# Optimization experiments

Measured on AMD Instinct MI355X. Metric: run time of the kernel, lower is better.

Reference implementation:

```python
import jax, jax.numpy as jnp
import numpy as np
from jax import lax

CENTER_VAR = 0.1
SIZE_VAR = 0.2
CONF_THR = 0.01
NMS_THR = 0.45
NMS_K = 100  # fixed candidate budget per (image, class) for jit-compatible NMS

B, N, C = 32, 24564, 81  # batch, priors (SSD512), classes incl. background


def setup_inputs() -> dict:
    key = jax.random.key(0)
    k1, k2, k3, k4 = jax.random.split(key, 4)
    cls_logits = jax.random.normal(k1, (B, N, C), dtype=jnp.float32)
    bbox_pred = jax.random.normal(k2, (B, N, 4), dtype=jnp.float32)
    # priors in center form (cx, cy, w, h), all in (0, 1)
    centers = jax.random.uniform(k3, (N, 2), dtype=jnp.float32)
    sizes = jax.random.uniform(k4, (N, 2), dtype=jnp.float32, minval=0.02, maxval=0.9)
    priors = jnp.concatenate([centers, sizes], axis=-1)
    return {"cls_logits": cls_logits, "bbox_pred": bbox_pred, "priors": priors}


def decode_boxes(locations, priors):
    # convert_locations_to_boxes (center form)
    cxcy = locations[..., :2] * CENTER_VAR * priors[..., 2:] + priors[..., :2]
    wh = jnp.exp(locations[..., 2:] * SIZE_VAR) * priors[..., 2:]
    # center_form_to_corner_form
    return jnp.concatenate([cxcy - wh / 2, cxcy + wh / 2], axis=-1)


def iou_matrix(boxes):
    # boxes: [K, 4] corner form -> [K, K] IoU
    lt = jnp.maximum(boxes[:, None, :2], boxes[None, :, :2])
    rb = jnp.minimum(boxes[:, None, 2:], boxes[None, :, 2:])
    wh = jnp.clip(rb - lt, 0.0)
    inter = wh[..., 0] * wh[..., 1]
    area = jnp.clip(boxes[:, 2] - boxes[:, 0], 0.0) * jnp.clip(boxes[:, 3] - boxes[:, 1], 0.0)
    return inter / (area[:, None] + area[None, :] - inter + 1e-8)


def greedy_nms(boxes, valid):
    # boxes [K,4] sorted by descending score; valid [K] bool (score > threshold)
    K = boxes.shape[0]
    iou = iou_matrix(boxes)
    idx = jnp.arange(K)

    def body(i, keep):
        suppress = (iou[i] > NMS_THR) & keep[i] & (idx > i)
        return keep & ~suppress

    keep = lax.fori_loop(0, K, body, valid)
    return keep


def reference(cls_logits, bbox_pred, priors):
    scores = jax.nn.softmax(cls_logits, axis=2)            # [B, N, C]
    boxes = decode_boxes(bbox_pred, priors)                # [B, N, 4]

    # --- post-processing: per-class top-k candidates + greedy NMS ---
    fg = jnp.transpose(scores[:, :, 1:], (0, 2, 1))        # [B, C-1, N]
    cand_scores, cand_idx = lax.top_k(fg, NMS_K)           # [B, C-1, K]
    cand_boxes = jnp.take_along_axis(boxes[:, None], cand_idx[..., None], axis=2)  # [B, C-1, K, 4]
    valid = cand_scores > CONF_THR

    keep = jax.vmap(jax.vmap(greedy_nms))(cand_boxes, valid)  # [B, C-1, K] bool
    nms_scores = jnp.where(keep, cand_scores, 0.0)
    nms_boxes = jnp.where(keep[..., None], cand_boxes, 0.0)
    return scores, boxes, nms_scores, nms_boxes, keep
```

## Files before the change

### kernel.cpp

```cpp
#include <hip/hip_runtime.h>
#include <hip/hip_bf16.h>
#include <math.h>

#define BB 32
#define NN 24564
#define CC 81
#define CM1 80
#define KK 100
#define CAP 512
#define CONF 0.01f
#define NMSTHR 0.45f

#define TROWS 64
#define TPB ((NN + TROWS - 1) / TROWS)

__device__ __forceinline__ float fexp_cr(float x) {
    return (float)exp((double)x);
}

__global__ __launch_bounds__(256) void softmax_kernel(const float* __restrict__ logits,
                                                      float* __restrict__ scores,
                                                      float* __restrict__ fg, int use_fg) {
#pragma clang fp contract(off)
    __shared__ __align__(16) float tile[TROWS * CC];
    __shared__ float sres[TROWS];

    const int blk = blockIdx.x;
    const int b = blk / TPB;
    const int t = blk - b * TPB;
    const int n0 = t * TROWS;
    int rows = NN - n0;
    if (rows > TROWS) rows = TROWS;
    const int tid = threadIdx.x;

    const float4* src4 = (const float4*)(logits + ((size_t)b * NN + n0) * CC);
    float4* tile4 = (float4*)tile;
    const int total4 = (rows * CC) >> 2;
    for (int i = tid; i < total4; i += 256) tile4[i] = src4[i];
    __syncthreads();

    if (tid < rows) {
        float* x = tile + tid * CC;
        float m = x[0];
        for (int c = 1; c < CC; ++c) m = fmaxf(m, x[c]);

        float r[8];
#pragma unroll
        for (int j = 0; j < 8; ++j) {
            float e = expf(x[j] - m);
            x[j] = e;
            r[j] = e;
        }
        for (int i = 8; i < 80; i += 8) {
#pragma unroll
            for (int j = 0; j < 8; ++j) {
                float e = expf(x[i + j] - m);
                x[i + j] = e;
                r[j] += e;
            }
        }
        float res = ((r[0] + r[1]) + (r[2] + r[3])) + ((r[4] + r[5]) + (r[6] + r[7]));
        float e80 = expf(x[80] - m);
        x[80] = e80;
        res += e80;
        sres[tid] = res;
    }
    __syncthreads();

    float4* dst4 = (float4*)(scores + ((size_t)b * NN + n0) * CC);
    for (int i = tid; i < total4; i += 256) {
        float4 v = tile4[i];
        int e0 = i << 2;
        unsigned r0 = (unsigned)(e0    ) / 81u;
        unsigned r1 = (unsigned)(e0 + 1) / 81u;
        unsigned r2 = (unsigned)(e0 + 2) / 81u;
        unsigned r3 = (unsigned)(e0 + 3) / 81u;
        v.x = v.x / sres[r0];
        v.y = v.y / sres[r1];
        v.z = v.z / sres[r2];
        v.w = v.w / sres[r3];
        dst4[i] = v;
        tile4[i] = v;
    }
    __syncthreads();

    if (use_fg) {
        const int rows4 = rows >> 2;
        for (int idx = tid; idx < CM1 * (TROWS >> 2); idx += 256) {
            int c  = idx >> 4;
            int j4 = idx & 15;
            if (j4 < rows4) {
                int j = j4 << 2;
                float4 v;
                v.x = tile[(j    ) * CC + (c + 1)];
                v.y = tile[(j + 1) * CC + (c + 1)];
                v.z = tile[(j + 2) * CC + (c + 1)];
                v.w = tile[(j + 3) * CC + (c + 1)];
                *(float4*)(fg + ((size_t)(b * CM1 + c)) * NN + n0 + j) = v;
            }
        }
    }
}

__global__ __launch_bounds__(256) void decode_kernel(const float* __restrict__ loc,
                                                     const float* __restrict__ priors,
                                                     float* __restrict__ boxes) {
#pragma clang fp contract(off)
    int row = blockIdx.x * 256 + threadIdx.x;
    if (row >= BB * NN) return;
    int n = row % NN;
    float4 L = ((const float4*)loc)[row];
    float4 P = ((const float4*)priors)[n];
    float cx = (L.x * 0.1f) * P.z + P.x;
    float cy = (L.y * 0.1f) * P.w + P.y;
    float w  = fexp_cr(L.z * 0.2f) * P.z;
    float h  = fexp_cr(L.w * 0.2f) * P.w;
    float4 o;
    o.x = cx - w * 0.5f;
    o.y = cy - h * 0.5f;
    o.z = cx + w * 0.5f;
    o.w = cy + h * 0.5f;
    ((float4*)boxes)[row] = o;
}

__global__ __launch_bounds__(256) void topk_nms_kernel(
    const float* __restrict__ scores, const float* __restrict__ fg, int use_fg,
    const float* __restrict__ boxes,
    float* __restrict__ nms_scores, float* __restrict__ nms_boxes,
    float* __restrict__ keep_out)
{
#pragma clang fp contract(off)
    const int blk = blockIdx.x;
    const int b = blk / CM1;
    const int c = blk - b * CM1;
    const int tid = threadIdx.x;

    __shared__ unsigned hist[4096];
    __shared__ unsigned partial[256];
    __shared__ unsigned long long cand[CAP];
    __shared__ unsigned scnt;
    __shared__ unsigned s_T;
    __shared__ int s_b1, s_above, s_refine;
    __shared__ float sbx[KK][4];
    __shared__ float sarea[KK];
    __shared__ float sscore[KK];
    __shared__ int skeep[KK];

    const float* src;
    size_t stride;
    if (use_fg) { src = fg + ((size_t)(b * CM1 + c)) * NN; stride = 1; }
    else        { src = scores + ((size_t)b * NN) * CC + (c + 1); stride = CC; }

    for (int i = tid; i < 4096; i += 256) hist[i] = 0u;
    __syncthreads();
    for (int n = tid; n < NN; n += 256) {
        unsigned bits = __float_as_uint(src[(size_t)n * stride]);
        atomicAdd(&hist[bits >> 20], 1u);
    }
    __syncthreads();
    unsigned psum = 0;
    for (int j = 0; j < 16; ++j) psum += hist[tid * 16 + j];
    partial[tid] = psum;
    __syncthreads();
    if (tid == 0) {
        unsigned acc = 0; int b1 = 0;
        for (int t = 255; t >= 0; --t) {
            if (acc + partial[t] >= (unsigned)KK) {
                for (int bin = t * 16 + 15; ; --bin) {
                    if (acc + hist[bin] >= (unsigned)KK) { b1 = bin; break; }
                    acc += hist[bin];
                }
                break;
            }
            acc += partial[t];
        }
        s_b1 = b1;
        s_above = (int)acc;
        s_refine = (acc + hist[b1] > CAP) ? 1 : 0;
        s_T = ((unsigned)b1) << 20;
    }
    __syncthreads();

    if (s_refine) {
        int b1 = s_b1;
        for (int i = tid; i < 4096; i += 256) hist[i] = 0u;
        __syncthreads();
        for (int n = tid; n < NN; n += 256) {
            unsigned bits = __float_as_uint(src[(size_t)n * stride]);
            if ((int)(bits >> 20) == b1) atomicAdd(&hist[(bits >> 8) & 0xFFFu], 1u);
        }
        __syncthreads();
        psum = 0;
        for (int j = 0; j < 16; ++j) psum += hist[tid * 16 + j];
        partial[tid] = psum;
        __syncthreads();
        if (tid == 0) {
            int K2 = KK - s_above;
            unsigned acc = 0; int b2 = 0;
            for (int t = 255; t >= 0; --t) {
                if ((int)(acc + partial[t]) >= K2) {
                    for (int bin = t * 16 + 15; ; --bin) {
                        if ((int)(acc + hist[bin]) >= K2) { b2 = bin; break; }
                        acc += hist[bin];
                    }
                    break;
                }
                acc += partial[t];
            }
            s_T = (((unsigned)s_b1) << 20) | (((unsigned)b2) << 8);
        }
        __syncthreads();
    }

    if (tid == 0) scnt = 0u;
    __syncthreads();
    unsigned T = s_T;
    for (int n = tid; n < NN; n += 256) {
        unsigned bits = __float_as_uint(src[(size_t)n * stride]);
        if (bits >= T) {
            unsigned pos = atomicAdd(&scnt, 1u);
            if (pos < CAP) {
                cand[pos] = (((unsigned long long)bits) << 32)
                          | (unsigned)(0xFFFFFFFFu - (unsigned)n);
            }
        }
    }
    __syncthreads();
    unsigned cnt = scnt; if (cnt > CAP) cnt = CAP;
    for (int i = tid; i < CAP; i += 256) {
        if ((unsigned)i >= cnt) cand[i] = 0ull;
    }
    __syncthreads();

    for (unsigned k = 2; k <= CAP; k <<= 1) {
        for (unsigned j = k >> 1; j > 0; j >>= 1) {
            for (unsigned e = tid; e < CAP; e += 256) {
                unsigned ixj = e ^ j;
                if (ixj > e) {
                    unsigned long long a = cand[e], bb2 = cand[ixj];
                    bool desc = ((e & k) == 0);
                    if (desc ? (a < bb2) : (a > bb2)) { cand[e] = bb2; cand[ixj] = a; }
                }
            }
            __syncthreads();
        }
    }

    if (tid < KK) {
        unsigned long long key = cand[tid];
        unsigned bits = (unsigned)(key >> 32);
        unsigned n = 0xFFFFFFFFu - (unsigned)(key & 0xFFFFFFFFu);
        float s = __uint_as_float(bits);
        sscore[tid] = s;
        skeep[tid] = (s > CONF) ? 1 : 0;
        float4 bx = ((const float4*)boxes)[(size_t)b * NN + n];
        sbx[tid][0] = bx.x; sbx[tid][1] = bx.y; sbx[tid][2] = bx.z; sbx[tid][3] = bx.w;
        sarea[tid] = fmaxf(bx.z - bx.x, 0.f) * fmaxf(bx.w - bx.y, 0.f);
    }
    __syncthreads();

    for (int i = 0; i < KK - 1; ++i) {
        if (skeep[i]) {
            int j = i + 1 + tid;
            if (j < KK) {
                float xx1 = fmaxf(sbx[i][0], sbx[j][0]);
                float yy1 = fmaxf(sbx[i][1], sbx[j][1]);
                float xx2 = fminf(sbx[i][2], sbx[j][2]);
                float yy2 = fminf(sbx[i][3], sbx[j][3]);
                float w = fmaxf(xx2 - xx1, 0.f);
                float h = fmaxf(yy2 - yy1, 0.f);
                float inter = w * h;
                float den = ((sarea[i] + sarea[j]) - inter) + 1e-8f;
                if (inter / den > NMSTHR) skeep[j] = 0;
            }
        }
        __syncthreads();
    }

    if (tid < KK) {
        int kf = skeep[tid];
        size_t oidx = (size_t)blk * KK + tid;
        nms_scores[oidx] = kf ? sscore[tid] : 0.f;
        keep_out[oidx]   = kf ? 1.f : 0.f;
        float4 ob;
        ob.x = kf ? sbx[tid][0] : 0.f;
        ob.y = kf ? sbx[tid][1] : 0.f;
        ob.z = kf ? sbx[tid][2] : 0.f;
        ob.w = kf ? sbx[tid][3] : 0.f;
        ((float4*)nms_boxes)[oidx] = ob;
    }
}

extern "C" void kernel_launch(void* const* d_in, const int* in_sizes, int n_in,
                              void* d_out, int out_size, void* d_ws, size_t ws_size,
                              hipStream_t stream) {
    const float* logits = (const float*)d_in[0];
    const float* bbox   = (const float*)d_in[1];
    const float* priors = (const float*)d_in[2];

    float* out = (float*)d_out;
    float* scores     = out;
    float* boxes      = scores + (size_t)BB * NN * CC;
    float* nms_scores = boxes + (size_t)BB * NN * 4;
    float* nms_boxes  = nms_scores + (size_t)BB * CM1 * KK;
    float* keep_out   = nms_boxes + (size_t)BB * CM1 * KK * 4;

    size_t fg_bytes = (size_t)BB * CM1 * NN * sizeof(float);
    int use_fg = (ws_size >= fg_bytes) ? 1 : 0;
    float* fg = (float*)d_ws;

    int rows = BB * NN;
    int blocksA = (rows + 255) / 256;
    softmax_kernel<<<BB * TPB, 256, 0, stream>>>(logits, scores, fg, use_fg);
    decode_kernel<<<blocksA, 256, 0, stream>>>(bbox, priors, boxes);
    topk_nms_kernel<<<BB * CM1, 256, 0, stream>>>(scores, fg, use_fg, boxes,
                                                  nms_scores, nms_boxes, keep_out);
}
```

Measured before the change: 814.9 us.

## Rework top-k NMS kernel with wave-level selection, register bitonic sort, ballot NMS

Result: faster. 692.2 us (-15.1%).

```diff
diff --git a/kernel.cpp b/kernel.cpp
--- a/kernel.cpp
+++ b/kernel.cpp
@@ -7,7 +7,7 @@
 #define CC 81
 #define CM1 80
 #define KK 100
-#define CAP 512
+#define CAP 256
 #define CONF 0.01f
 #define NMSTHR 0.45f
 
@@ -123,6 +123,46 @@
     ((float4*)boxes)[row] = o;
 }
 
+__device__ __forceinline__ unsigned wave_suffix_incl(unsigned x, int lane) {
+#pragma unroll
+    for (int d = 1; d < 64; d <<= 1) {
+        unsigned t = __shfl_down(x, d);
+        if (lane + d < 64) x += t;
+    }
+    return x;
+}
+
+struct BinSel { int bin; int above; int cnt; int found; };
+
+__device__ __forceinline__ BinSel wave_select_bin(const unsigned* hist,
+                                                  const unsigned* partial,
+                                                  int lane, unsigned Ktarget) {
+    BinSel r;
+    unsigned g = partial[4 * lane] + partial[4 * lane + 1]
+               + partial[4 * lane + 2] + partial[4 * lane + 3];
+    unsigned S = wave_suffix_incl(g, lane);
+    unsigned total = __shfl(S, 0);
+    if (total < Ktarget) { r.bin = -1; r.above = 0; r.cnt = 0; r.found = 0; return r; }
+    unsigned Sn = __shfl_down(S, 1);
+    if (lane == 63) Sn = 0u;
+    bool ok = (S >= Ktarget) && (Sn < Ktarget);
+    unsigned long long m = __ballot(ok);
+    int lstar = __ffsll((unsigned long long)m) - 1;
+    unsigned above_g = __shfl(Sn, lstar);
+    unsigned h = hist[(lstar << 6) + lane];
+    unsigned S2 = wave_suffix_incl(h, lane);
+    unsigned S2n = __shfl_down(S2, 1);
+    if (lane == 63) S2n = 0u;
+    bool ok2 = (above_g + S2 >= Ktarget) && (above_g + S2n < Ktarget);
+    unsigned long long m2 = __ballot(ok2);
+    int l2 = __ffsll(m2) - 1;
+    r.bin = (lstar << 6) + l2;
+    r.above = (int)(above_g + __shfl(S2n, l2));
+    r.cnt = (int)__shfl(h, l2);
+    r.found = 1;
+    return r;
+}
+
 __global__ __launch_bounds__(256) void topk_nms_kernel(
     const float* __restrict__ scores, const float* __restrict__ fg, int use_fg,
     const float* __restrict__ boxes,
@@ -134,148 +174,226 @@
     const int b = blk / CM1;
     const int c = blk - b * CM1;
     const int tid = threadIdx.x;
-
-    __shared__ unsigned hist[4096];
+    const int lane = tid & 63;
+    const int wave = tid >> 6;
+
+    __shared__ __align__(16) unsigned hist[4096];
     __shared__ unsigned partial[256];
-    __shared__ unsigned long long cand[CAP];
     __shared__ unsigned scnt;
     __shared__ unsigned s_T;
     __shared__ int s_b1, s_above, s_refine;
-    __shared__ float sbx[KK][4];
-    __shared__ float sarea[KK];
-    __shared__ float sscore[KK];
-    __shared__ int skeep[KK];
-
-    const float* src;
-    size_t stride;
-    if (use_fg) { src = fg + ((size_t)(b * CM1 + c)) * NN; stride = 1; }
-    else        { src = scores + ((size_t)b * NN) * CC + (c + 1); stride = CC; }
-
-    for (int i = tid; i < 4096; i += 256) hist[i] = 0u;
-    __syncthreads();
-    for (int n = tid; n < NN; n += 256) {
-        unsigned bits = __float_as_uint(src[(size_t)n * stride]);
-        atomicAdd(&hist[bits >> 20], 1u);
-    }
-    __syncthreads();
-    unsigned psum = 0;
-    for (int j = 0; j < 16; ++j) psum += hist[tid * 16 + j];
-    partial[tid] = psum;
-    __syncthreads();
-    if (tid == 0) {
-        unsigned acc = 0; int b1 = 0;
-        for (int t = 255; t >= 0; --t) {
-            if (acc + partial[t] >= (unsigned)KK) {
-                for (int bin = t * 16 + 15; ; --bin) {
-                    if (acc + hist[bin] >= (unsigned)KK) { b1 = bin; break; }
-                    acc += hist[bin];
+
+    unsigned long long* cand = (unsigned long long*)hist;
+    float (*sbx)[4] = (float (*)[4])(hist + 512);
+    float* sarea  = (float*)(hist + 912);
+    float* sscore = (float*)(hist + 1012);
+    int*   skeep  = (int*)(hist + 1112);
+
+    const unsigned CONFB = __float_as_uint(CONF);
+
+    const float* src = use_fg ? (fg + ((size_t)(b * CM1 + c)) * NN)
+                              : (scores + ((size_t)b * NN) * CC + (c + 1));
+
+    uint4* h4z = (uint4*)hist;
+    const uint4 z4 = make_uint4(0u, 0u, 0u, 0u);
+    for (int i = tid; i < 1024; i += 256) h4z[i] = z4;
+    __syncthreads();
+
+    if (use_fg) {
+        const float4* s4 = (const float4*)src;
+        for (int i = tid; i < NN / 4; i += 256) {
+            float4 v = s4[i];
+            unsigned q0 = __float_as_uint(v.x), q1 = __float_as_uint(v.y);
+            unsigned q2 = __float_as_uint(v.z), q3 = __float_as_uint(v.w);
+            if (q0 > CONFB) atomicAdd(&hist[q0 >> 20], 1u);
+            if (q1 > CONFB) atomicAdd(&hist[q1 >> 20], 1u);
+            if (q2 > CONFB) atomicAdd(&hist[q2 >> 20], 1u);
+            if (q3 > CONFB) atomicAdd(&hist[q3 >> 20], 1u);
+        }
+    } else {
+        for (int n = tid; n < NN; n += 256) {
+            unsigned bits = __float_as_uint(src[(size_t)n * CC]);
+            if (bits > CONFB) atomicAdd(&hist[bits >> 20], 1u);
+        }
+    }
+    __syncthreads();
+
+    {
+        const uint4* h4 = (const uint4*)hist;
+        unsigned s = 0;
+#pragma unroll
+        for (int q = 0; q < 4; ++q) {
+            uint4 u = h4[tid * 4 + q];
+            s += u.x + u.y + u.z + u.w;
+        }
+        partial[tid] = s;
+    }
+    __syncthreads();
+
+    if (tid < 64) {
+        BinSel r = wave_select_bin(hist, partial, lane, (unsigned)KK);
+        if (lane == 0) {
+            scnt = 0u;
+            if (!r.found) {
+                s_T = 0u; s_refine = 0; s_b1 = -1; s_above = 0;
+            } else {
+                s_b1 = r.bin; s_above = r.above;
+                s_refine = (r.above + r.cnt > CAP) ? 1 : 0;
+                s_T = ((unsigned)r.bin) << 20;
+            }
+        }
+    }
+    __syncthreads();
+
+    if (s_refine) {
+        const int b1 = s_b1;
+        for (int i = tid; i < 1024; i += 256) h4z[i] = z4;
+        __syncthreads();
+        if (use_fg) {
+            const float4* s4 = (const float4*)src;
+            for (int i = tid; i < NN / 4; i += 256) {
+                float4 v = s4[i];
+                unsigned qq[4] = {__float_as_uint(v.x), __float_as_uint(v.y),
+                                  __float_as_uint(v.z), __float_as_uint(v.w)};
+#pragma unroll
+                for (int q = 0; q < 4; ++q)
+                    if (qq[q] > CONFB && (int)(qq[q] >> 20) == b1)
+                        atomicAdd(&hist[(qq[q] >> 8) & 0xFFFu], 1u);
+            }
+        } else {
+            for (int n = tid; n < NN; n += 256) {
+                unsigned bits = __float_as_uint(src[(size_t)n * CC]);
+                if (bits > CONFB && (int)(bits >> 20) == b1)
+                    atomicAdd(&hist[(bits >> 8) & 0xFFFu], 1u);
+            }
+        }
+        __syncthreads();
+        {
+            const uint4* h4 = (const uint4*)hist;
+            unsigned s = 0;
+#pragma unroll
+            for (int q = 0; q < 4; ++q) {
+                uint4 u = h4[tid * 4 + q];
+                s += u.x + u.y + u.z + u.w;
+            }
+            partial[tid] = s;
+        }
+        __syncthreads();
+        if (tid < 64) {
+            BinSel r2 = wave_select_bin(hist, partial, lane, (unsigned)(KK - s_above));
+            if (lane == 0 && r2.found)
+                s_T = (((unsigned)s_b1) << 20) | (((unsigned)r2.bin) << 8);
+        }
+        __syncthreads();
+    }
+
+    const unsigned T = s_T;
+    if (use_fg) {
+        const float4* s4 = (const float4*)src;
+        for (int i = tid; i < NN / 4; i += 256) {
+            float4 v = s4[i];
+            unsigned qq[4] = {__float_as_uint(v.x), __float_as_uint(v.y),
+                              __float_as_uint(v.z), __float_as_uint(v.w)};
+#pragma unroll
+            for (int q = 0; q < 4; ++q) {
+                unsigned bits = qq[q];
+                if (bits > CONFB && bits >= T) {
+                    unsigned pos = atomicAdd(&scnt, 1u);
+                    if (pos < CAP)
+                        cand[pos] = (((unsigned long long)bits) << 32)
+                                  | (unsigned)(0xFFFFFFFFu - (unsigned)(i * 4 + q));
                 }
-                break;
-            }
-            acc += partial[t];
-        }
-        s_b1 = b1;
-        s_above = (int)acc;
-        s_refine = (acc + hist[b1] > CAP) ? 1 : 0;
-        s_T = ((unsigned)b1) << 20;
-    }
-    __syncthreads();
-
-    if (s_refine) {
-        int b1 = s_b1;
-        for (int i = tid; i < 4096; i += 256) hist[i] = 0u;
-        __syncthreads();
+            }
+        }
+    } else {
         for (int n = tid; n < NN; n += 256) {
-            unsigned bits = __float_as_uint(src[(size_t)n * stride]);
-            if ((int)(bits >> 20) == b1) atomicAdd(&hist[(bits >> 8) & 0xFFFu], 1u);
-        }
-        __syncthreads();
-        psum = 0;
-        for (int j = 0; j < 16; ++j) psum += hist[tid * 16 + j];
-        partial[tid] = psum;
-        __syncthreads();
-        if (tid == 0) {
-            int K2 = KK - s_above;
-            unsigned acc = 0; int b2 = 0;
-            for (int t = 255; t >= 0; --t) {
-                if ((int)(acc + partial[t]) >= K2) {
-                    for (int bin = t * 16 + 15; ; --bin) {
-                        if ((int)(acc + hist[bin]) >= K2) { b2 = bin; break; }
-                        acc += hist[bin];
-                    }
-                    break;
-                }
-                acc += partial[t];
-            }
-            s_T = (((unsigned)s_b1) << 20) | (((unsigned)b2) << 8);
-        }
-        __syncthreads();
-    }
-
-    if (tid == 0) scnt = 0u;
-    __syncthreads();
-    unsigned T = s_T;
-    for (int n = tid; n < NN; n += 256) {
-        unsigned bits = __float_as_uint(src[(size_t)n * stride]);
-        if (bits >= T) {
-            unsigned pos = atomicAdd(&scnt, 1u);
-            if (pos < CAP) {
-                cand[pos] = (((unsigned long long)bits) << 32)
-                          | (unsigned)(0xFFFFFFFFu - (unsigned)n);
+            unsigned bits = __float_as_uint(src[(size_t)n * CC]);
+            if (bits > CONFB && bits >= T) {
+                unsigned pos = atomicAdd(&scnt, 1u);
+                if (pos < CAP)
+                    cand[pos] = (((unsigned long long)bits) << 32)
+                              | (unsigned)(0xFFFFFFFFu - (unsigned)n);
             }
         }
     }
     __syncthreads();
     unsigned cnt = scnt; if (cnt > CAP) cnt = CAP;
-    for (int i = tid; i < CAP; i += 256) {
-        if ((unsigned)i >= cnt) cand[i] = 0ull;
-    }
-    __syncthreads();
-
-    for (unsigned k = 2; k <= CAP; k <<= 1) {
+    if ((unsigned)tid >= cnt) cand[tid] = 0ull;
+    __syncthreads();
+
+    unsigned long long v = cand[tid];
+    for (unsigned k = 2; k <= 256; k <<= 1) {
         for (unsigned j = k >> 1; j > 0; j >>= 1) {
-            for (unsigned e = tid; e < CAP; e += 256) {
-                unsigned ixj = e ^ j;
-                if (ixj > e) {
-                    unsigned long long a = cand[e], bb2 = cand[ixj];
-                    bool desc = ((e & k) == 0);
-                    if (desc ? (a < bb2) : (a > bb2)) { cand[e] = bb2; cand[ixj] = a; }
-                }
-            }
-            __syncthreads();
-        }
-    }
+            unsigned long long p;
+            if (j >= 64) {
+                __syncthreads();
+                cand[tid] = v;
+                __syncthreads();
+                p = cand[tid ^ j];
+            } else {
+                p = __shfl_xor(v, (int)j, 64);
+            }
+            bool keep_max = (((tid & j) == 0u) == ((tid & k) == 0u));
+            bool take = ((p > v) == keep_max);
+            v = take ? p : v;
+        }
+    }
+    __syncthreads();
 
     if (tid < KK) {
-        unsigned long long key = cand[tid];
-        unsigned bits = (unsigned)(key >> 32);
-        unsigned n = 0xFFFFFFFFu - (unsigned)(key & 0xFFFFFFFFu);
-        float s = __uint_as_float(bits);
-        sscore[tid] = s;
-        skeep[tid] = (s > CONF) ? 1 : 0;
-        float4 bx = ((const float4*)boxes)[(size_t)b * NN + n];
-        sbx[tid][0] = bx.x; sbx[tid][1] = bx.y; sbx[tid][2] = bx.z; sbx[tid][3] = bx.w;
-        sarea[tid] = fmaxf(bx.z - bx.x, 0.f) * fmaxf(bx.w - bx.y, 0.f);
-    }
-    __syncthreads();
-
-    for (int i = 0; i < KK - 1; ++i) {
-        if (skeep[i]) {
-            int j = i + 1 + tid;
-            if (j < KK) {
-                float xx1 = fmaxf(sbx[i][0], sbx[j][0]);
-                float yy1 = fmaxf(sbx[i][1], sbx[j][1]);
-                float xx2 = fminf(sbx[i][2], sbx[j][2]);
-                float yy2 = fminf(sbx[i][3], sbx[j][3]);
-                float w = fmaxf(xx2 - xx1, 0.f);
-                float h = fmaxf(yy2 - yy1, 0.f);
-                float inter = w * h;
-                float den = ((sarea[i] + sarea[j]) - inter) + 1e-8f;
-                if (inter / den > NMSTHR) skeep[j] = 0;
-            }
-        }
-        __syncthreads();
-    }
+        unsigned bits = (unsigned)(v >> 32);
+        if (bits != 0u) {
+            unsigned n = 0xFFFFFFFFu - (unsigned)(v & 0xFFFFFFFFu);
+            float s = __uint_as_float(bits);
+            sscore[tid] = s;
+            skeep[tid] = (s > CONF) ? 1 : 0;
+            float4 bx = ((const float4*)boxes)[(size_t)b * NN + n];
+            sbx[tid][0] = bx.x; sbx[tid][1] = bx.y; sbx[tid][2] = bx.z; sbx[tid][3] = bx.w;
+            sarea[tid] = fmaxf(bx.z - bx.x, 0.f) * fmaxf(bx.w - bx.y, 0.f);
+        } else {
+            sscore[tid] = 0.f; skeep[tid] = 0;
+            sbx[tid][0] = 0.f; sbx[tid][1] = 0.f; sbx[tid][2] = 0.f; sbx[tid][3] = 0.f;
+            sarea[tid] = 0.f;
+        }
+    }
+    __syncthreads();
+
+    if (wave == 0) {
+        const int j1 = lane + 64;
+        const bool hasj1 = (j1 < KK);
+        float4 B0 = make_float4(sbx[lane][0], sbx[lane][1], sbx[lane][2], sbx[lane][3]);
+        float a0 = sarea[lane];
+        float4 B1 = hasj1 ? make_float4(sbx[j1][0], sbx[j1][1], sbx[j1][2], sbx[j1][3])
+                          : make_float4(0.f, 0.f, 0.f, 0.f);
+        float a1 = hasj1 ? sarea[j1] : 0.f;
+        unsigned long long k0 = __ballot(skeep[lane] != 0);
+        unsigned long long k1 = __ballot(hasj1 && skeep[j1] != 0);
+        for (int i = 0; i < KK - 1; ++i) {
+            bool alive = (i < 64) ? ((k0 >> i) & 1ull) : ((k1 >> (i - 64)) & 1ull);
+            if (!alive) continue;
+            float bix = sbx[i][0], biy = sbx[i][1], biz = sbx[i][2], biw = sbx[i][3];
+            float ai = sarea[i];
+            float xx1 = fmaxf(bix, B0.x), yy1 = fmaxf(biy, B0.y);
+            float xx2 = fminf(biz, B0.z), yy2 = fminf(biw, B0.w);
+            float w0 = fmaxf(xx2 - xx1, 0.f), h0 = fmaxf(yy2 - yy1, 0.f);
+            float inter0 = w0 * h0;
+            float den0 = ((ai + a0) - inter0) + 1e-8f;
+            bool s0 = (lane > i) && (inter0 / den0 > NMSTHR);
+            float xb1 = fmaxf(bix, B1.x), yb1 = fmaxf(biy, B1.y);
+            float xb2 = fminf(biz, B1.z), yb2 = fminf(biw, B1.w);
+            float wb = fmaxf(xb2 - xb1, 0.f), hb = fmaxf(yb2 - yb1, 0.f);
+            float interb = wb * hb;
+            float denb = ((ai + a1) - interb) + 1e-8f;
+            bool s1 = hasj1 && (j1 > i) && (interb / denb > NMSTHR);
+            unsigned long long sup0 = __ballot(s0);
+            unsigned long long sup1 = __ballot(s1);
+            k0 &= ~sup0;
+            k1 &= ~sup1;
+        }
+        skeep[lane] = (int)((k0 >> lane) & 1ull);
+        if (hasj1) skeep[j1] = (int)((k1 >> lane) & 1ull);
+    }
+    __syncthreads();
 
     if (tid < KK) {
         int kf = skeep[tid];
```
